# Performance work log

Hardware: AMD Instinct MI355X
Metric: run time of the kernel (lower is better)

## Reference

```python
import jax, jax.numpy as jnp
import numpy as np

N_NODES = 100_000
N_EDGES = 1_600_000  # avg degree 16
D_FEAT = 64


def setup_inputs() -> dict:
    key = jax.random.key(0)
    k_x, k_val, k_src, k_dst = jax.random.split(key, 4)
    x = jax.random.normal(k_x, (N_NODES, D_FEAT), dtype=jnp.float32)
    edge_val = jax.random.uniform(k_val, (N_EDGES,), dtype=jnp.float32)
    edge_src = jax.random.randint(k_src, (N_EDGES,), 0, N_NODES, dtype=jnp.int32)
    edge_dst = jax.random.randint(k_dst, (N_EDGES,), 0, N_NODES, dtype=jnp.int32)
    return {"x": x, "edge_val": edge_val, "edge_src": edge_src, "edge_dst": edge_dst}


def reference(x, edge_val, edge_src, edge_dst):
    # out = adj @ x  with adj in COO form:
    # out[dst] += val * x[src]   (sparse-dense matmul, SpMM)
    msgs = x[edge_src] * edge_val[:, None]          # [E, D] gather + scale
    out = jax.ops.segment_sum(msgs, edge_dst, num_segments=N_NODES)  # [N, D] scatter-add
    return out
```

## Files before the change

### kernel.cpp

```cpp
#include <hip/hip_runtime.h>

#define N_NODES 100000
#define N_EDGES 1600000
#define D_FEAT 64
#define NPB 128
#define K_BUCKETS 782
#define CAP 2304
#define A_BLOCKS 800
#define A_CHUNK 2000
#define A_THREADS 512
#define S_THREADS 512

__global__ __launch_bounds__(A_THREADS) void scatterA(
        const int* __restrict__ src, const int* __restrict__ dst,
        const float* __restrict__ val, int* __restrict__ cursor,
        int2* __restrict__ bdata) {
    __shared__ int sh_cnt[K_BUCKETS];
    __shared__ int sh_base[K_BUCKETS];
    for (int i = threadIdx.x; i < K_BUCKETS; i += A_THREADS) sh_cnt[i] = 0;
    __syncthreads();
    const int base = blockIdx.x * A_CHUNK;
    for (int j = threadIdx.x; j < A_CHUNK; j += A_THREADS)
        atomicAdd(&sh_cnt[dst[base + j] >> 7], 1);
    __syncthreads();
    for (int i = threadIdx.x; i < K_BUCKETS; i += A_THREADS) {
        const int c = sh_cnt[i];
        sh_base[i] = c ? (i * CAP + atomicAdd(&cursor[i], c)) : 0;
    }
    __syncthreads();
    for (int i = threadIdx.x; i < K_BUCKETS; i += A_THREADS) sh_cnt[i] = 0;
    __syncthreads();
    for (int j = threadIdx.x; j < A_CHUNK; j += A_THREADS) {
        const int e = base + j;
        const int d = dst[e];
        const int b = d >> 7;
        const int slot = atomicAdd(&sh_cnt[b], 1);
        bdata[sh_base[b] + slot] =
            make_int2(src[e] | ((d & 127) << 17), __float_as_int(val[e]));
    }
}

__global__ __launch_bounds__(S_THREADS) void sort_spmm(
        const float* __restrict__ x, const int2* __restrict__ bdata,
        const int* __restrict__ cursor, float* __restrict__ out) {
    __shared__ int2 sh_e[CAP];
    __shared__ int2 sh_s[CAP];
    __shared__ int cnt[NPB];
    __shared__ int cur[NPB];
    const int b = blockIdx.x;
    const int count = min(cursor[b], CAP);
    const int base = b * CAP;
    const int t = threadIdx.x;

    if (t < NPB) cnt[t] = 0;
    __syncthreads();
    for (int j = t; j < count; j += S_THREADS) {
        const int2 e = bdata[base + j];
        sh_e[j] = e;
        atomicAdd(&cnt[e.x >> 17], 1);
    }
    __syncthreads();
    const int v = (t < NPB) ? cnt[t] : 0;
    for (int off = 1; off < NPB; off <<= 1) {
        int u = 0;
        if (t < NPB && t >= off) u = cnt[t - off];
        __syncthreads();
        if (t < NPB) cnt[t] += u;
        __syncthreads();
    }
    if (t < NPB) cur[t] = cnt[t] - v;
    __syncthreads();
    for (int j = t; j < count; j += S_THREADS) {
        const int2 pv = sh_e[j];
        const int dl = pv.x >> 17;
        const int slot = atomicAdd(&cur[dl], 1);
        sh_s[slot] = make_int2(pv.x & 0x1FFFF, pv.y);
    }
    __syncthreads();

    const int lane = t & 15;
    const int rg = t >> 4;
    const int row0 = b * NPB;
    for (int r = rg; r < NPB; r += S_THREADS / 16) {
        const int node = row0 + r;
        if (node >= N_NODES) continue;
        const int beg = r ? cnt[r - 1] : 0;
        const int end = cnt[r];
        float4 acc = {0.f, 0.f, 0.f, 0.f};
        int j = beg;
        for (; j + 4 <= end; j += 4) {
            const int2 p0 = sh_s[j];
            const int2 p1 = sh_s[j + 1];
            const int2 p2 = sh_s[j + 2];
            const int2 p3 = sh_s[j + 3];
            const float4 m0 = ((const float4*)(x + (size_t)p0.x * D_FEAT))[lane];
            const float4 m1 = ((const float4*)(x + (size_t)p1.x * D_FEAT))[lane];
            const float4 m2 = ((const float4*)(x + (size_t)p2.x * D_FEAT))[lane];
            const float4 m3 = ((const float4*)(x + (size_t)p3.x * D_FEAT))[lane];
            const float v0 = __int_as_float(p0.y);
            const float v1 = __int_as_float(p1.y);
            const float v2 = __int_as_float(p2.y);
            const float v3 = __int_as_float(p3.y);
            acc.x += v0 * m0.x + v1 * m1.x + v2 * m2.x + v3 * m3.x;
            acc.y += v0 * m0.y + v1 * m1.y + v2 * m2.y + v3 * m3.y;
            acc.z += v0 * m0.z + v1 * m1.z + v2 * m2.z + v3 * m3.z;
            acc.w += v0 * m0.w + v1 * m1.w + v2 * m2.w + v3 * m3.w;
        }
        for (; j < end; ++j) {
            const int2 p0 = sh_s[j];
            const float4 m0 = ((const float4*)(x + (size_t)p0.x * D_FEAT))[lane];
            const float v0 = __int_as_float(p0.y);
            acc.x += v0 * m0.x;
            acc.y += v0 * m0.y;
            acc.z += v0 * m0.z;
            acc.w += v0 * m0.w;
        }
        ((float4*)(out + (size_t)node * D_FEAT))[lane] = acc;
    }
}

extern "C" void kernel_launch(void* const* d_in, const int* in_sizes, int n_in,
                              void* d_out, int out_size, void* d_ws, size_t ws_size,
                              hipStream_t stream) {
    const float* x        = (const float*)d_in[0];
    const float* edge_val = (const float*)d_in[1];
    const int*   edge_src = (const int*)d_in[2];
    const int*   edge_dst = (const int*)d_in[3];
    float* out = (float*)d_out;

    int* ws     = (int*)d_ws;
    int* cursor = ws;
    int2* bdata = (int2*)(ws + K_BUCKETS);

    hipMemsetAsync(cursor, 0, K_BUCKETS * sizeof(int), stream);

    scatterA <<<A_BLOCKS, A_THREADS, 0, stream>>>(edge_src, edge_dst, edge_val,
                                                  cursor, bdata);
    sort_spmm<<<K_BUCKETS, S_THREADS, 0, stream>>>(x, bdata, cursor, out);
}
```

Before: 190.0 us.

## Stage bucketed edges in LDS for coalesced writes and use nontemporal memory ops

```diff
diff --git a/kernel.cpp b/kernel.cpp
--- a/kernel.cpp
+++ b/kernel.cpp
@@ -6,37 +6,75 @@
 #define NPB 128
 #define K_BUCKETS 782
 #define CAP 2304
-#define A_BLOCKS 800
-#define A_CHUNK 2000
+#define A_BLOCKS 400
+#define A_CHUNK 4000
 #define A_THREADS 512
-#define S_THREADS 512
+#define S_THREADS 256
+
+typedef long long i64;
+typedef float f4 __attribute__((ext_vector_type(4)));
 
 __global__ __launch_bounds__(A_THREADS) void scatterA(
         const int* __restrict__ src, const int* __restrict__ dst,
         const float* __restrict__ val, int* __restrict__ cursor,
         int2* __restrict__ bdata) {
-    __shared__ int sh_cnt[K_BUCKETS];
-    __shared__ int sh_base[K_BUCKETS];
-    for (int i = threadIdx.x; i < K_BUCKETS; i += A_THREADS) sh_cnt[i] = 0;
+    __shared__ int cnt[K_BUCKETS];
+    __shared__ int lstart[K_BUCKETS];
+    __shared__ int adj[K_BUCKETS];
+    __shared__ int cur[K_BUCKETS];
+    __shared__ int sums[A_THREADS];
+    __shared__ int2 staged[A_CHUNK];
+    __shared__ int gidx[A_CHUNK];
+    const int t = threadIdx.x;
+    const int base = blockIdx.x * A_CHUNK;
+
+    for (int i = t; i < K_BUCKETS; i += A_THREADS) cnt[i] = 0;
     __syncthreads();
-    const int base = blockIdx.x * A_CHUNK;
-    for (int j = threadIdx.x; j < A_CHUNK; j += A_THREADS)
-        atomicAdd(&sh_cnt[dst[base + j] >> 7], 1);
+    for (int j = t; j < A_CHUNK; j += A_THREADS)
+        atomicAdd(&cnt[dst[base + j] >> 7], 1);
     __syncthreads();
-    for (int i = threadIdx.x; i < K_BUCKETS; i += A_THREADS) {
-        const int c = sh_cnt[i];
-        sh_base[i] = c ? (i * CAP + atomicAdd(&cursor[i], c)) : 0;
+
+    int s0 = 0, s1 = 0;
+    if (t < K_BUCKETS / 2) { s0 = cnt[2 * t]; s1 = cnt[2 * t + 1]; }
+    sums[t] = s0 + s1;
+    __syncthreads();
+    for (int off = 1; off < A_THREADS; off <<= 1) {
+        const int u = (t >= off) ? sums[t - off] : 0;
+        __syncthreads();
+        sums[t] += u;
+        __syncthreads();
+    }
+    if (t < K_BUCKETS / 2) {
+        const int excl = sums[t] - (s0 + s1);
+        lstart[2 * t]     = excl;
+        lstart[2 * t + 1] = excl + s0;
     }
     __syncthreads();
-    for (int i = threadIdx.x; i < K_BUCKETS; i += A_THREADS) sh_cnt[i] = 0;
+
+    for (int i = t; i < K_BUCKETS; i += A_THREADS) {
+        const int c = cnt[i];
+        const int ls = lstart[i];
+        cur[i] = ls;
+        adj[i] = c ? (i * CAP + atomicAdd(&cursor[i], c)) - ls : 0;
+    }
     __syncthreads();
-    for (int j = threadIdx.x; j < A_CHUNK; j += A_THREADS) {
+
+    for (int j = t; j < A_CHUNK; j += A_THREADS) {
         const int e = base + j;
         const int d = dst[e];
         const int b = d >> 7;
-        const int slot = atomicAdd(&sh_cnt[b], 1);
-        bdata[sh_base[b] + slot] =
-            make_int2(src[e] | ((d & 127) << 17), __float_as_int(val[e]));
+        const int s = __builtin_nontemporal_load(src + e);
+        const float v = __builtin_nontemporal_load(val + e);
+        const int r = atomicAdd(&cur[b], 1);
+        staged[r] = make_int2(s | ((d & 127) << 17), __float_as_int(v));
+        gidx[r] = adj[b] + r;
+    }
+    __syncthreads();
+
+    for (int j = t; j < A_CHUNK; j += A_THREADS) {
+        const int2 pv = staged[j];
+        const i64 raw = (i64)(unsigned)pv.x | ((i64)pv.y << 32);
+        __builtin_nontemporal_store(raw, (i64*)(bdata + gidx[j]));
     }
 }
 
@@ -55,7 +93,8 @@
     if (t < NPB) cnt[t] = 0;
     __syncthreads();
     for (int j = t; j < count; j += S_THREADS) {
-        const int2 e = bdata[base + j];
+        const i64 raw = __builtin_nontemporal_load((const i64*)(bdata + base + j));
+        const int2 e = make_int2((int)(unsigned)raw, (int)(raw >> 32));
         sh_e[j] = e;
         atomicAdd(&cnt[e.x >> 17], 1);
     }
@@ -115,7 +154,8 @@
             acc.z += v0 * m0.z;
             acc.w += v0 * m0.w;
         }
-        ((float4*)(out + (size_t)node * D_FEAT))[lane] = acc;
+        const f4 accv = {acc.x, acc.y, acc.z, acc.w};
+        __builtin_nontemporal_store(accv, (f4*)(out + (size_t)node * D_FEAT) + lane);
     }
 }
 
```

After: 171.1 us. 10.0% less time.
